# Kernel tuning notes

Hardware: AMD Instinct MI355X
Metric: run time of the kernel (lower is better)

Reference implementation:

```python
import jax, jax.numpy as jnp
import numpy as np


def setup_inputs() -> dict:
    key = jax.random.key(0)
    k1, k2 = jax.random.split(key)
    B, N, M, D = 32, 2048, 2048, 3
    x = jax.random.normal(k1, (B, N, D), dtype=jnp.float32)
    y = jax.random.normal(k2, (B, M, D), dtype=jnp.float32)
    return {"x": x, "y": y}


def reference(x, y):
    # x: [B, N, D], y: [B, M, D]
    # dist[b, m, n] = ||x[b, n] - y[b, m]||^2  -> [B, M, N]
    diff = x[:, None, :, :] - y[:, :, None, :]          # [B, M, N, D]
    dist = jnp.sum(diff * diff, axis=-1)                # [B, M, N]
    # min over M (axis 1): for each x-point, nearest y-point; mean over N
    row = jnp.mean(jnp.min(dist, axis=1), axis=-1)      # [B]
    # min over N (axis 2): for each y-point, nearest x-point; mean over M
    col = jnp.mean(jnp.min(dist, axis=2), axis=-1)      # [B]
    # per-batch max of the two directed means, then mean over batch
    return jnp.mean(jnp.maximum(row, col))
```

## Files before the change

### kernel.cpp

```cpp
#include <hip/hip_runtime.h>


#define BATCH   32
#define NPTS    2048
#define THREADS 128
#define QPT     16
#define TCH     32
#define TC      (NPTS / TCH)
#define NSEG    (2 * BATCH)
#define CTHREADS 256
#define CBLK    8
#define NCOMB   (NSEG * CBLK)

__global__ __launch_bounds__(THREADS, 4) void chamfer_min(
    const float* __restrict__ x, const float* __restrict__ y,
    float* __restrict__ part )
{
    __shared__ float4 t4[TC];

    const int blk   = blockIdx.x;
    const int dir   = blk >> 10;
    const int r     = blk & 1023;
    const int b     = r >> 5;
    const int chunk = r & 31;

    const float* q = (dir == 0 ? x : y) + (size_t)b * NPTS * 3;
    const float* t = (dir == 0 ? y : x) + (size_t)b * NPTS * 3;

    if (threadIdx.x < TC) {
        int jj = chunk * TC + threadIdx.x;
        float tx = t[3 * jj + 0];
        float ty = t[3 * jj + 1];
        float tz = t[3 * jj + 2];
        t4[threadIdx.x] = make_float4(tx, ty, tz, 0.5f * (tx * tx + ty * ty + tz * tz));
    }

    float nqx[QPT], nqy[QPT], nqz[QPT], mn[QPT];
#pragma unroll
    for (int k = 0; k < QPT; ++k) {
        int qi = threadIdx.x + k * THREADS;
        nqx[k] = -q[3 * qi + 0];
        nqy[k] = -q[3 * qi + 1];
        nqz[k] = -q[3 * qi + 2];
        mn[k]  = 3.4e38f;
    }
    __syncthreads();

#pragma unroll 2
    for (int j = 0; j < TC; j += 2) {
        float4 a = t4[j];
        float4 c = t4[j + 1];
#pragma unroll
        for (int k = 0; k < QPT; ++k) {
            float s0 = fmaf(nqz[k], a.z, fmaf(nqy[k], a.y, fmaf(nqx[k], a.x, a.w)));
            float s1 = fmaf(nqz[k], c.z, fmaf(nqy[k], c.y, fmaf(nqx[k], c.x, c.w)));
            mn[k] = fminf(fminf(mn[k], s0), s1);
        }
    }

    float* pbase = part + ((size_t)(dir * BATCH + b) * TCH + chunk) * NPTS;
#pragma unroll
    for (int k = 0; k < QPT; ++k)
        pbase[threadIdx.x + k * THREADS] = mn[k];
}

__global__ __launch_bounds__(CTHREADS) void chamfer_combine(
    const float* __restrict__ x, const float* __restrict__ y,
    const float* __restrict__ part,
    float* __restrict__ blocksums )
{
    __shared__ float wsum[CTHREADS / 64];

    const int blk = blockIdx.x;
    const int seg = blk >> 3;
    const int qc  = blk & 7;
    const int dir = seg >> 5;
    const int b   = seg & 31;
    const int qi  = qc * CTHREADS + threadIdx.x;

    const float* p = part + (size_t)seg * TCH * NPTS + qi;
    float mn = p[0];
#pragma unroll
    for (int c = 1; c < TCH; ++c)
        mn = fminf(mn, p[(size_t)c * NPTS]);

    const float* q = (dir == 0 ? x : y) + (size_t)b * NPTS * 3 + 3 * qi;
    float qx = q[0], qy = q[1], qz = q[2];
    float d = fmaf(2.0f, mn, qx * qx + qy * qy + qz * qz);

    for (int off = 32; off > 0; off >>= 1)
        d += __shfl_down(d, off);
    if ((threadIdx.x & 63) == 0) wsum[threadIdx.x >> 6] = d;
    __syncthreads();
    if (threadIdx.x == 0)
        blocksums[blk] = wsum[0] + wsum[1] + wsum[2] + wsum[3];
}

__global__ void chamfer_finalize(const float* __restrict__ blocksums,
                                 float* __restrict__ out)
{
    const int lane = threadIdx.x;
    float s = 0.0f;
#pragma unroll
    for (int i = 0; i < CBLK; ++i)
        s += blocksums[lane * CBLK + i];
    float other = __shfl(s, lane + 32);
    float v = (lane < 32) ? fmaxf(s, other) * (1.0f / NPTS) : 0.0f;
    for (int off = 16; off > 0; off >>= 1)
        v += __shfl_down(v, off);
    if (lane == 0) out[0] = v * (1.0f / BATCH);
}

extern "C" void kernel_launch(void* const* d_in, const int* in_sizes, int n_in,
                              void* d_out, int out_size, void* d_ws, size_t ws_size,
                              hipStream_t stream) {
    const float* x = (const float*)d_in[0];
    const float* y = (const float*)d_in[1];
    float* out = (float*)d_out;

    float* part      = (float*)d_ws;
    float* blocksums = part + (size_t)NSEG * TCH * NPTS;

    chamfer_min<<<2 * BATCH * TCH, THREADS, 0, stream>>>(x, y, part);
    chamfer_combine<<<NCOMB, CTHREADS, 0, stream>>>(x, y, part, blocksums);
    chamfer_finalize<<<1, 64, 0, stream>>>(blocksums, out);
}
```

Before: 86.79 us.

## Compute row and column minima from one distance pass instead of two directions

Instead of running the pairwise distance pass twice (x→y and y→x), each block computes full squared distances once. It keeps the per-query row minima as before and also reduces column minima across threads through shared memory. This halves the FMA work and drops the second direction's partial buffer. In exchange it adds a per-column reduction through a 128×33 LDS array, extra adds per pair, and more shared memory per block, which may lower occupancy.

```diff
diff --git a/kernel.cpp b/kernel.cpp
--- a/kernel.cpp
+++ b/kernel.cpp
@@ -5,43 +5,47 @@
 #define NPTS    2048
 #define THREADS 128
 #define QPT     16
-#define TCH     32
+#define TCH     64
 #define TC      (NPTS / TCH)
-#define NSEG    (2 * BATCH)
-#define CTHREADS 256
-#define CBLK    8
-#define NCOMB   (NSEG * CBLK)
+#define NROWB   (BATCH * 8)
+#define NCOLB   BATCH
 
 __global__ __launch_bounds__(THREADS, 4) void chamfer_min(
     const float* __restrict__ x, const float* __restrict__ y,
-    float* __restrict__ part )
+    float* __restrict__ part    ,
+    float* __restrict__ colmin  )
 {
     __shared__ float4 t4[TC];
+    __shared__ float colLds[THREADS][TC + 1];
+    __shared__ float cmPart[4][TC + 1];
 
     const int blk   = blockIdx.x;
-    const int dir   = blk >> 10;
-    const int r     = blk & 1023;
-    const int b     = r >> 5;
-    const int chunk = r & 31;
+    const int b     = blk >> 6;
+    const int chunk = blk & 63;
 
-    const float* q = (dir == 0 ? x : y) + (size_t)b * NPTS * 3;
-    const float* t = (dir == 0 ? y : x) + (size_t)b * NPTS * 3;
+    const float* qp = x + (size_t)b * NPTS * 3;
+    const float* tp = y + (size_t)b * NPTS * 3;
 
     if (threadIdx.x < TC) {
         int jj = chunk * TC + threadIdx.x;
-        float tx = t[3 * jj + 0];
-        float ty = t[3 * jj + 1];
-        float tz = t[3 * jj + 2];
-        t4[threadIdx.x] = make_float4(tx, ty, tz, 0.5f * (tx * tx + ty * ty + tz * tz));
+        float ty0 = tp[3 * jj + 0];
+        float ty1 = tp[3 * jj + 1];
+        float ty2 = tp[3 * jj + 2];
+        t4[threadIdx.x] = make_float4(ty0, ty1, ty2,
+                                      0.5f * (ty0 * ty0 + ty1 * ty1 + ty2 * ty2));
     }
 
-    float nqx[QPT], nqy[QPT], nqz[QPT], mn[QPT];
+    float nqx[QPT], nqy[QPT], nqz[QPT], hx[QPT], mn[QPT];
 #pragma unroll
     for (int k = 0; k < QPT; ++k) {
         int qi = threadIdx.x + k * THREADS;
-        nqx[k] = -q[3 * qi + 0];
-        nqy[k] = -q[3 * qi + 1];
-        nqz[k] = -q[3 * qi + 2];
+        float qx = qp[3 * qi + 0];
+        float qy = qp[3 * qi + 1];
+        float qz = qp[3 * qi + 2];
+        nqx[k] = -qx;
+        nqy[k] = -qy;
+        nqz[k] = -qz;
+        hx[k]  = 0.5f * (qx * qx + qy * qy + qz * qz);
         mn[k]  = 3.4e38f;
     }
     __syncthreads();
@@ -49,44 +53,80 @@
 #pragma unroll 2
     for (int j = 0; j < TC; j += 2) {
         float4 a = t4[j];
-        float4 c = t4[j + 1];
+        float4 c4 = t4[j + 1];
+        float colA = 3.4e38f, colB = 3.4e38f;
 #pragma unroll
-        for (int k = 0; k < QPT; ++k) {
-            float s0 = fmaf(nqz[k], a.z, fmaf(nqy[k], a.y, fmaf(nqx[k], a.x, a.w)));
-            float s1 = fmaf(nqz[k], c.z, fmaf(nqy[k], c.y, fmaf(nqx[k], c.x, c.w)));
-            mn[k] = fminf(fminf(mn[k], s0), s1);
+        for (int k = 0; k < QPT; k += 2) {
+            float Wa0 = a.w  + hx[k],     Wb0 = c4.w + hx[k];
+            float Wa1 = a.w  + hx[k + 1], Wb1 = c4.w + hx[k + 1];
+            float s0 = fmaf(nqz[k], a.z, fmaf(nqy[k], a.y, fmaf(nqx[k], a.x, Wa0)));
+            float s1 = fmaf(nqz[k], c4.z, fmaf(nqy[k], c4.y, fmaf(nqx[k], c4.x, Wb0)));
+            float t0 = fmaf(nqz[k+1], a.z, fmaf(nqy[k+1], a.y, fmaf(nqx[k+1], a.x, Wa1)));
+            float t1 = fmaf(nqz[k+1], c4.z, fmaf(nqy[k+1], c4.y, fmaf(nqx[k+1], c4.x, Wb1)));
+            mn[k]     = fminf(fminf(mn[k], s0), s1);
+            mn[k + 1] = fminf(fminf(mn[k + 1], t0), t1);
+            colA = fminf(fminf(colA, s0), t0);
+            colB = fminf(fminf(colB, s1), t1);
         }
+        colLds[threadIdx.x][j]     = colA;
+        colLds[threadIdx.x][j + 1] = colB;
+    }
+    __syncthreads();
+
+    {
+        const int g = threadIdx.x >> 5;
+        const int j = threadIdx.x & 31;
+        float cp = 3.4e38f;
+#pragma unroll
+        for (int i = 0; i < 32; ++i)
+            cp = fminf(cp, colLds[g * 32 + i][j]);
+        cmPart[g][j] = cp;
+    }
+    __syncthreads();
+    if (threadIdx.x < TC) {
+        const int j = threadIdx.x;
+        float cm = fminf(fminf(cmPart[0][j], cmPart[1][j]),
+                         fminf(cmPart[2][j], cmPart[3][j]));
+        colmin[(size_t)b * NPTS + chunk * TC + j] = cm;
     }
 
-    float* pbase = part + ((size_t)(dir * BATCH + b) * TCH + chunk) * NPTS;
+    float* pbase = part + ((size_t)b * TCH + chunk) * NPTS;
 #pragma unroll
     for (int k = 0; k < QPT; ++k)
         pbase[threadIdx.x + k * THREADS] = mn[k];
 }
 
+#define CTHREADS 256
+
 __global__ __launch_bounds__(CTHREADS) void chamfer_combine(
-    const float* __restrict__ x, const float* __restrict__ y,
     const float* __restrict__ part,
+    const float* __restrict__ colmin,
     float* __restrict__ blocksums )
 {
     __shared__ float wsum[CTHREADS / 64];
 
     const int blk = blockIdx.x;
-    const int seg = blk >> 3;
-    const int qc  = blk & 7;
-    const int dir = seg >> 5;
-    const int b   = seg & 31;
-    const int qi  = qc * CTHREADS + threadIdx.x;
+    float d;
 
-    const float* p = part + (size_t)seg * TCH * NPTS + qi;
-    float mn = p[0];
+    if (blk < NROWB) {
+        const int b  = blk >> 3;
+        const int qc = blk & 7;
+        const int qi = qc * CTHREADS + threadIdx.x;
+        const float* p = part + (size_t)b * TCH * NPTS + qi;
+        float mn = p[0];
 #pragma unroll
-    for (int c = 1; c < TCH; ++c)
-        mn = fminf(mn, p[(size_t)c * NPTS]);
-
-    const float* q = (dir == 0 ? x : y) + (size_t)b * NPTS * 3 + 3 * qi;
-    float qx = q[0], qy = q[1], qz = q[2];
-    float d = fmaf(2.0f, mn, qx * qx + qy * qy + qz * qz);
+        for (int c = 1; c < TCH; ++c)
+            mn = fminf(mn, p[(size_t)c * NPTS]);
+        d = 2.0f * mn;
+    } else {
+        const int b = blk - NROWB;
+        const float* p = colmin + (size_t)b * NPTS;
+        float s = 0.0f;
+#pragma unroll
+        for (int i = 0; i < 8; ++i)
+            s += p[threadIdx.x + i * CTHREADS];
+        d = 2.0f * s;
+    }
 
     for (int off = 32; off > 0; off >>= 1)
         d += __shfl_down(d, off);
@@ -100,13 +140,16 @@
                                  float* __restrict__ out)
 {
     const int lane = threadIdx.x;
-    float s = 0.0f;
+    float v = 0.0f;
+    if (lane < BATCH) {
+        float rs = 0.0f;
 #pragma unroll
-    for (int i = 0; i < CBLK; ++i)
-        s += blocksums[lane * CBLK + i];
-    float other = __shfl(s, lane + 32);
-    float v = (lane < 32) ? fmaxf(s, other) * (1.0f / NPTS) : 0.0f;
-    for (int off = 16; off > 0; off >>= 1)
+        for (int i = 0; i < 8; ++i)
+            rs += blocksums[lane * 8 + i];
+        float cs = blocksums[NROWB + lane];
+        v = fmaxf(rs, cs) * (1.0f / NPTS);
+    }
+    for (int off = 32; off > 0; off >>= 1)
         v += __shfl_down(v, off);
     if (lane == 0) out[0] = v * (1.0f / BATCH);
 }
@@ -119,9 +162,10 @@
     float* out = (float*)d_out;
 
     float* part      = (float*)d_ws;
-    float* blocksums = part + (size_t)NSEG * TCH * NPTS;
+    float* colmin    = part + (size_t)BATCH * TCH * NPTS;
+    float* blocksums = colmin + (size_t)BATCH * NPTS;
 
-    chamfer_min<<<2 * BATCH * TCH, THREADS, 0, stream>>>(x, y, part);
-    chamfer_combine<<<NCOMB, CTHREADS, 0, stream>>>(x, y, part, blocksums);
+    chamfer_min<<<BATCH * TCH, THREADS, 0, stream>>>(x, y, part, colmin);
+    chamfer_combine<<<NROWB + NCOLB, CTHREADS, 0, stream>>>(part, colmin, blocksums);
     chamfer_finalize<<<1, 64, 0, stream>>>(blocksums, out);
 }
```

Measured after the change: 84.21 us. 1.03x faster.
